# Kernel tuning notes

Measured on AMD Instinct MI355X. Metric: run time of the kernel, lower is better.

## Reference

```python
import jax, jax.numpy as jnp
import numpy as np

B, C, H, W = 16, 21, 512, 512


def setup_inputs() -> dict:
    key = jax.random.key(0)
    k1, k2 = jax.random.split(key)
    # y_pred: class probabilities (softmax over class dim of random logits)
    logits = jax.random.normal(k1, (B, C, H, W), dtype=jnp.float32)
    y_pred = jax.nn.softmax(logits, axis=1)
    # y_true: one-hot ground truth built from random integer labels
    labels = jax.random.randint(k2, (B, H, W), 0, C)
    y_true = jax.nn.one_hot(labels, C, axis=1, dtype=jnp.float32)  # [B,C,H,W]
    return {"y_pred": y_pred, "y_true": y_true, "bg": 0}


def reference(y_pred, y_true, bg):
    eps = 1e-11
    # static slice: classes l in [bg, C)
    yt = y_true[:, bg:]  # [B, C', H, W]
    yp = y_pred[:, bg:]
    ta = jnp.sum(yt, axis=(2, 3))            # [B, C'] target mass per class
    tb = jnp.sum(yp, axis=(2, 3))            # [B, C'] pred mass per class
    inter = jnp.sum(yt * yp, axis=(2, 3))    # [B, C'] intersection
    valid = ta != 0                          # classes skipped when target empty
    dice = jnp.where(valid, 2.0 * inter / (ta + tb + eps), 0.0)
    cpt2 = jnp.sum(valid, axis=1).astype(jnp.float32)  # [B] non-empty classes
    denom = cpt2 - bg                        # matches original cpt2 - bg divisor
    batch_valid = denom != 0
    safe_denom = jnp.where(batch_valid, denom, 1.0)
    tmp = jnp.where(batch_valid, jnp.sum(dice, axis=1) / safe_denom, 0.0)  # [B]
    cpt1 = jnp.sum(batch_valid).astype(jnp.float32)
    loss = 1.0 - jnp.sum(tmp) / jnp.maximum(cpt1, 1.0)
    return jnp.where(cpt1 > 0, loss, jnp.float32(-1.0))
```

## Files before the change

kernel.cpp:

```cpp
#include <hip/hip_runtime.h>


#define BB 16
#define CC 21
#define HW (512 * 512)
#define SPLIT 16
#define CHUNK (HW / SPLIT)
#define NBC (BB * CC)
#define NPART (NBC * SPLIT)

typedef float floatx4 __attribute__((ext_vector_type(4)));

__global__ __launch_bounds__(256) void dice_reduce_kernel(
    const float* __restrict__ y_pred,
    const float* __restrict__ y_true,
    const int* __restrict__ bg_ptr,
    float* __restrict__ part)
{
    const int blk   = blockIdx.x;
    const int split = blk % SPLIT;
    const int bc    = blk / SPLIT;
    const int c     = bc % CC;
    const int bg    = *bg_ptr;
    if (c < bg) return;

    const size_t base = (size_t)bc * HW + (size_t)split * CHUNK;
    const floatx4* __restrict__ p4 = (const floatx4*)(y_pred + base);
    const floatx4* __restrict__ t4 = (const floatx4*)(y_true + base);

    float st = 0.0f, sp = 0.0f, stp = 0.0f;
    const int tid = threadIdx.x;

    #pragma unroll 8
    for (int k = 0; k < (CHUNK / 4) / 256; ++k) {
        const int i = tid + k * 256;
        floatx4 p = __builtin_nontemporal_load(&p4[i]);
        floatx4 t = __builtin_nontemporal_load(&t4[i]);
        sp  += (p.x + p.y) + (p.z + p.w);
        st  += (t.x + t.y) + (t.z + t.w);
        stp += (t.x * p.x + t.y * p.y) + (t.z * p.z + t.w * p.w);
    }

    #pragma unroll
    for (int off = 32; off > 0; off >>= 1) {
        st  += __shfl_down(st,  off, 64);
        sp  += __shfl_down(sp,  off, 64);
        stp += __shfl_down(stp, off, 64);
    }

    __shared__ float sm[3][4];
    const int wave = tid >> 6;
    const int lane = tid & 63;
    if (lane == 0) { sm[0][wave] = st; sm[1][wave] = sp; sm[2][wave] = stp; }
    __syncthreads();

    if (tid == 0) {
        part[0 * NPART + blk] = (sm[0][0] + sm[0][1]) + (sm[0][2] + sm[0][3]);
        part[1 * NPART + blk] = (sm[1][0] + sm[1][1]) + (sm[1][2] + sm[1][3]);
        part[2 * NPART + blk] = (sm[2][0] + sm[2][1]) + (sm[2][2] + sm[2][3]);
    }
}

__global__ __launch_bounds__(384) void dice_final_kernel(
    const float* __restrict__ part,
    const int* __restrict__ bg_ptr,
    float* __restrict__ out)
{
    const float eps = 1e-11f;
    const int bg = *bg_ptr;
    __shared__ float dice_sum[BB];
    __shared__ int   valid_cnt[BB];

    const int tid = threadIdx.x;
    if (tid < BB) { dice_sum[tid] = 0.0f; valid_cnt[tid] = 0; }
    __syncthreads();

    if (tid < NBC) {
        const int c = tid % CC;
        const int b = tid / CC;
        if (c >= bg) {
            float ta = 0.0f, tb = 0.0f, inter = 0.0f;
            #pragma unroll
            for (int s = 0; s < SPLIT; s++) {
                ta    += part[0 * NPART + tid * SPLIT + s];
                tb    += part[1 * NPART + tid * SPLIT + s];
                inter += part[2 * NPART + tid * SPLIT + s];
            }
            if (ta != 0.0f) {
                float dice = 2.0f * inter / (ta + tb + eps);
                atomicAdd(&dice_sum[b], dice);
                atomicAdd(&valid_cnt[b], 1);
            }
        }
    }
    __syncthreads();

    if (tid == 0) {
        float sum_tmp = 0.0f;
        int cpt1 = 0;
        for (int b = 0; b < BB; b++) {
            float denom = (float)valid_cnt[b] - (float)bg;
            if (denom != 0.0f) {
                sum_tmp += dice_sum[b] / denom;
                cpt1++;
            }
        }
        float loss = 1.0f - sum_tmp / fmaxf((float)cpt1, 1.0f);
        out[0] = (cpt1 > 0) ? loss : -1.0f;
    }
}

extern "C" void kernel_launch(void* const* d_in, const int* in_sizes, int n_in,
                              void* d_out, int out_size, void* d_ws, size_t ws_size,
                              hipStream_t stream) {
    const float* y_pred = (const float*)d_in[0];
    const float* y_true = (const float*)d_in[1];
    const int*   bg_ptr = (const int*)d_in[2];
    float* out  = (float*)d_out;
    float* part = (float*)d_ws;

    dice_reduce_kernel<<<NBC * SPLIT, 256, 0, stream>>>(y_pred, y_true, bg_ptr, part);
    dice_final_kernel<<<1, 384, 0, stream>>>(part, bg_ptr, out);
}
```

Before: 619.1 us.

## Flatten reduction over all planes with fixed block count and plane-tagged partials

The reduction no longer splits each (batch, class) plane into a fixed number of chunks. It divides the whole flattened input evenly across 2048 blocks, so each block may straddle two planes and keeps two sets of accumulators. Each block writes two records tagged with a plane index, and the final kernel scatters them into shared per-plane sums with atomics. The aim is a block count that fills the GPU evenly. The cost is a per-element branch, extra accumulators, and no longer skipping planes below bg.

Result: slower. 633.9 us (+2.4%).

```diff
diff --git a/kernel.cpp b/kernel.cpp
--- a/kernel.cpp
+++ b/kernel.cpp
@@ -4,90 +4,114 @@
 #define BB 16
 #define CC 21
 #define HW (512 * 512)
-#define SPLIT 16
-#define CHUNK (HW / SPLIT)
-#define NBC (BB * CC)
-#define NPART (NBC * SPLIT)
+#define NPLANES (BB * CC)
+#define HW_F4 (HW / 4)
+#define TOTAL_F4 (NPLANES * HW_F4)
+#define NBLK 2048
+#define PER_BLK (TOTAL_F4 / NBLK)
+#define PER_THREAD (PER_BLK / 256)
+#define NREC (NBLK * 2)
 
 typedef float floatx4 __attribute__((ext_vector_type(4)));
 
 __global__ __launch_bounds__(256) void dice_reduce_kernel(
     const float* __restrict__ y_pred,
     const float* __restrict__ y_true,
-    const int* __restrict__ bg_ptr,
     float* __restrict__ part)
 {
-    const int blk   = blockIdx.x;
-    const int split = blk % SPLIT;
-    const int bc    = blk / SPLIT;
-    const int c     = bc % CC;
-    const int bg    = *bg_ptr;
-    if (c < bg) return;
-
-    const size_t base = (size_t)bc * HW + (size_t)split * CHUNK;
-    const floatx4* __restrict__ p4 = (const floatx4*)(y_pred + base);
-    const floatx4* __restrict__ t4 = (const floatx4*)(y_true + base);
-
-    float st = 0.0f, sp = 0.0f, stp = 0.0f;
+    const int blk = blockIdx.x;
     const int tid = threadIdx.x;
 
-    #pragma unroll 8
-    for (int k = 0; k < (CHUNK / 4) / 256; ++k) {
+    const size_t f4base = (size_t)blk * PER_BLK;
+    const floatx4* __restrict__ p4 = (const floatx4*)y_pred + f4base;
+    const floatx4* __restrict__ t4 = (const floatx4*)y_true + f4base;
+
+    const int p0 = (int)(f4base >> 16);
+    const int p1 = (int)((f4base + PER_BLK - 1) >> 16);
+    const size_t rem = (((size_t)(p0 + 1)) << 16) - f4base;
+    const int bound = rem < (size_t)PER_BLK ? (int)rem : PER_BLK;
+
+    float st0 = 0.f, sp0 = 0.f, stp0 = 0.f;
+    float st1 = 0.f, sp1 = 0.f, stp1 = 0.f;
+
+    #pragma unroll 7
+    for (int k = 0; k < PER_THREAD; ++k) {
         const int i = tid + k * 256;
         floatx4 p = __builtin_nontemporal_load(&p4[i]);
         floatx4 t = __builtin_nontemporal_load(&t4[i]);
-        sp  += (p.x + p.y) + (p.z + p.w);
-        st  += (t.x + t.y) + (t.z + t.w);
-        stp += (t.x * p.x + t.y * p.y) + (t.z * p.z + t.w * p.w);
+        const float s_p  = (p.x + p.y) + (p.z + p.w);
+        const float s_t  = (t.x + t.y) + (t.z + t.w);
+        const float s_tp = (t.x * p.x + t.y * p.y) + (t.z * p.z + t.w * p.w);
+        if (i < bound) { sp0 += s_p; st0 += s_t; stp0 += s_tp; }
+        else           { sp1 += s_p; st1 += s_t; stp1 += s_tp; }
     }
 
     #pragma unroll
     for (int off = 32; off > 0; off >>= 1) {
-        st  += __shfl_down(st,  off, 64);
-        sp  += __shfl_down(sp,  off, 64);
-        stp += __shfl_down(stp, off, 64);
+        st0  += __shfl_down(st0,  off, 64);
+        sp0  += __shfl_down(sp0,  off, 64);
+        stp0 += __shfl_down(stp0, off, 64);
+        st1  += __shfl_down(st1,  off, 64);
+        sp1  += __shfl_down(sp1,  off, 64);
+        stp1 += __shfl_down(stp1, off, 64);
     }
 
-    __shared__ float sm[3][4];
+    __shared__ float sm[6][4];
     const int wave = tid >> 6;
     const int lane = tid & 63;
-    if (lane == 0) { sm[0][wave] = st; sm[1][wave] = sp; sm[2][wave] = stp; }
+    if (lane == 0) {
+        sm[0][wave] = st0; sm[1][wave] = sp0; sm[2][wave] = stp0;
+        sm[3][wave] = st1; sm[4][wave] = sp1; sm[5][wave] = stp1;
+    }
     __syncthreads();
 
     if (tid == 0) {
-        part[0 * NPART + blk] = (sm[0][0] + sm[0][1]) + (sm[0][2] + sm[0][3]);
-        part[1 * NPART + blk] = (sm[1][0] + sm[1][1]) + (sm[1][2] + sm[1][3]);
-        part[2 * NPART + blk] = (sm[2][0] + sm[2][1]) + (sm[2][2] + sm[2][3]);
+        float r0 = (sm[0][0] + sm[0][1]) + (sm[0][2] + sm[0][3]);
+        float r1 = (sm[1][0] + sm[1][1]) + (sm[1][2] + sm[1][3]);
+        float r2 = (sm[2][0] + sm[2][1]) + (sm[2][2] + sm[2][3]);
+        float r3 = (sm[3][0] + sm[3][1]) + (sm[3][2] + sm[3][3]);
+        float r4 = (sm[4][0] + sm[4][1]) + (sm[4][2] + sm[4][3]);
+        float r5 = (sm[5][0] + sm[5][1]) + (sm[5][2] + sm[5][3]);
+        floatx4* rec = (floatx4*)part;
+        floatx4 a; a.x = r0; a.y = r1; a.z = r2; a.w = (float)p0;
+        floatx4 b; b.x = r3; b.y = r4; b.z = r5; b.w = (float)p1;
+        rec[blk * 2 + 0] = a;
+        rec[blk * 2 + 1] = b;
     }
 }
 
-__global__ __launch_bounds__(384) void dice_final_kernel(
+__global__ __launch_bounds__(512) void dice_final_kernel(
     const float* __restrict__ part,
     const int* __restrict__ bg_ptr,
     float* __restrict__ out)
 {
     const float eps = 1e-11f;
-    const int bg = *bg_ptr;
+    __shared__ float ta_s[NPLANES], tb_s[NPLANES], in_s[NPLANES];
     __shared__ float dice_sum[BB];
     __shared__ int   valid_cnt[BB];
 
     const int tid = threadIdx.x;
-    if (tid < BB) { dice_sum[tid] = 0.0f; valid_cnt[tid] = 0; }
+    for (int i = tid; i < NPLANES; i += 512) { ta_s[i] = 0.f; tb_s[i] = 0.f; in_s[i] = 0.f; }
+    if (tid < BB) { dice_sum[tid] = 0.f; valid_cnt[tid] = 0; }
     __syncthreads();
 
-    if (tid < NBC) {
+    for (int r = tid; r < NREC; r += 512) {
+        floatx4 rec = *(const floatx4*)(part + (size_t)r * 4);
+        const int pl = (int)rec.w;
+        atomicAdd(&ta_s[pl], rec.x);
+        atomicAdd(&tb_s[pl], rec.y);
+        atomicAdd(&in_s[pl], rec.z);
+    }
+    __syncthreads();
+
+    const int bg = *bg_ptr;
+    if (tid < NPLANES) {
         const int c = tid % CC;
         const int b = tid / CC;
         if (c >= bg) {
-            float ta = 0.0f, tb = 0.0f, inter = 0.0f;
-            #pragma unroll
-            for (int s = 0; s < SPLIT; s++) {
-                ta    += part[0 * NPART + tid * SPLIT + s];
-                tb    += part[1 * NPART + tid * SPLIT + s];
-                inter += part[2 * NPART + tid * SPLIT + s];
-            }
+            const float ta = ta_s[tid];
             if (ta != 0.0f) {
-                float dice = 2.0f * inter / (ta + tb + eps);
+                const float dice = 2.0f * in_s[tid] / (ta + tb_s[tid] + eps);
                 atomicAdd(&dice_sum[b], dice);
                 atomicAdd(&valid_cnt[b], 1);
             }
@@ -99,13 +123,13 @@
         float sum_tmp = 0.0f;
         int cpt1 = 0;
         for (int b = 0; b < BB; b++) {
-            float denom = (float)valid_cnt[b] - (float)bg;
+            const float denom = (float)valid_cnt[b] - (float)bg;
             if (denom != 0.0f) {
                 sum_tmp += dice_sum[b] / denom;
                 cpt1++;
             }
         }
-        float loss = 1.0f - sum_tmp / fmaxf((float)cpt1, 1.0f);
+        const float loss = 1.0f - sum_tmp / fmaxf((float)cpt1, 1.0f);
         out[0] = (cpt1 > 0) ? loss : -1.0f;
     }
 }
@@ -119,6 +143,6 @@
     float* out  = (float*)d_out;
     float* part = (float*)d_ws;
 
-    dice_reduce_kernel<<<NBC * SPLIT, 256, 0, stream>>>(y_pred, y_true, bg_ptr, part);
-    dice_final_kernel<<<1, 384, 0, stream>>>(part, bg_ptr, out);
+    dice_reduce_kernel<<<NBLK, 256, 0, stream>>>(y_pred, y_true, part);
+    dice_final_kernel<<<1, 512, 0, stream>>>(part, bg_ptr, out);
 }
```
